# Kernel optimization log

Hardware: AMD Instinct MI355X
Metric: run time of the kernel (lower is better)

## Reference

```python
import jax, jax.numpy as jnp
import numpy as np

N = 50000      # nodes
E = 800000     # edges (before self-loops)
IN, HID, HEADS, OUT = 128, 16, 8, 64
NEG_SLOPE = 0.2
EPS = 1e-16


def gat_layer(x, edge_index, W, att_src, att_dst, bias, heads, ch, num_nodes, concat):
    # x: [N, F_in]; edge_index: [2, E'] (row0 = source j, row1 = target i)
    h = (x @ W).reshape(-1, heads, ch)                     # [N, H, C]
    a_src = jnp.sum(h * att_src, axis=-1)                  # [N, H]
    a_dst = jnp.sum(h * att_dst, axis=-1)                  # [N, H]
    src, dst = edge_index[0], edge_index[1]
    alpha = a_src[src] + a_dst[dst]                        # [E', H]
    alpha = jax.nn.leaky_relu(alpha, NEG_SLOPE)
    # segment softmax over incoming edges of each target node
    m = jax.ops.segment_max(alpha, dst, num_segments=num_nodes)
    alpha = jnp.exp(alpha - m[dst])
    denom = jax.ops.segment_sum(alpha, dst, num_segments=num_nodes)
    alpha = alpha / (denom[dst] + EPS)
    msg = h[src] * alpha[:, :, None]                       # [E', H, C]
    out = jax.ops.segment_sum(msg, dst, num_segments=num_nodes)  # [N, H, C]
    out = out.reshape(-1, heads * ch) if concat else out.mean(axis=1)
    return out + bias


def gat_model(x, edge_index, W1, att_src1, att_dst1, b1, W2, att_src2, att_dst2, b2, num_nodes):
    # PyG GATConv default add_self_loops=True
    loops = jnp.arange(num_nodes, dtype=edge_index.dtype)
    ei = jnp.concatenate([edge_index, jnp.stack([loops, loops])], axis=1)
    h = gat_layer(x, ei, W1, att_src1, att_dst1, b1, HEADS, HID, num_nodes, concat=True)
    h = jax.nn.relu(h)
    return gat_layer(h, ei, W2, att_src2, att_dst2, b2, 1, OUT, num_nodes, concat=False)


def setup_inputs() -> dict:
    key = jax.random.key(0)
    ks = jax.random.split(key, 10)
    x = jax.random.normal(ks[0], (N, IN), jnp.float32)
    edge_index = jax.random.randint(ks[1], (2, E), 0, N, dtype=jnp.int32)
    W1 = jax.random.normal(ks[2], (IN, HEADS * HID), jnp.float32) / np.sqrt(IN).astype(np.float32)
    att_src1 = jax.random.normal(ks[3], (HEADS, HID), jnp.float32) * 0.1
    att_dst1 = jax.random.normal(ks[4], (HEADS, HID), jnp.float32) * 0.1
    b1 = jnp.zeros((HEADS * HID,), jnp.float32)
    W2 = jax.random.normal(ks[5], (HEADS * HID, OUT), jnp.float32) / np.sqrt(HEADS * HID).astype(np.float32)
    att_src2 = jax.random.normal(ks[6], (1, OUT), jnp.float32) * 0.1
    att_dst2 = jax.random.normal(ks[7], (1, OUT), jnp.float32) * 0.1
    b2 = jnp.zeros((OUT,), jnp.float32)
    return {"x": x, "edge_index": edge_index, "W1": W1, "att_src1": att_src1,
            "att_dst1": att_dst1, "b1": b1, "W2": W2, "att_src2": att_src2,
            "att_dst2": att_dst2, "b2": b2, "num_nodes": N}


def reference(x, edge_index, W1, att_src1, att_dst1, b1, W2, att_src2, att_dst2, b2, num_nodes):
    return gat_model(x, edge_index, W1, att_src1, att_dst1, b1,
                     W2, att_src2, att_dst2, b2, num_nodes)
```

## Files before the change

### kernel.cpp

```cpp
#include <hip/hip_runtime.h>

#define NEG 0.2f
#define EPSV 1e-16f
#define EPB 4096
#define CAPN 64
#define CAPB (256 * 18)

typedef _Float16 h4 __attribute__((ext_vector_type(4)));
typedef _Float16 h8 __attribute__((ext_vector_type(8)));
typedef float f32x4 __attribute__((ext_vector_type(4)));

__device__ __forceinline__ float lrelu(float x) { return x > 0.f ? x : NEG * x; }

__global__ void k_setup(const float* __restrict__ W1, _Float16* __restrict__ Wt1,
                        const float* __restrict__ W2, _Float16* __restrict__ Wt2,
                        int* __restrict__ bcur, int nbuckets) {
  const int bid = blockIdx.x, tid = threadIdx.x;
  if (bid < 64) {
    int t = bid * 256 + tid;
    int c = t >> 7, k = t & 127;
    Wt1[t] = (_Float16)W1[k * 128 + c];
  } else if (bid < 96) {
    int t = (bid - 64) * 256 + tid;
    if (t < 64 * 128) {
      int c = t >> 7, k = t & 127;
      Wt2[t] = (_Float16)W2[k * 64 + c];
    }
  } else {
    if (tid < nbuckets) bcur[tid] = tid * CAPB;
  }
}

__global__ __launch_bounds__(256) void k_bin_gemm1(
    const int* __restrict__ src, const int* __restrict__ dst, int* __restrict__ bcur,
    unsigned* __restrict__ binned, int E, int nBinB, const float* __restrict__ X,
    const _Float16* __restrict__ Wt, const float* __restrict__ atts,
    const float* __restrict__ attd, _Float16* __restrict__ Hout,
    float* __restrict__ as_, float* __restrict__ ad_, int N) {
  constexpr int K = 128, XS = 136;
  __shared__ _Float16 xs[64 * XS];
  const int tid = threadIdx.x;

  if ((int)blockIdx.x < nBinB) {
    int* hist = (int*)xs;
    int* base = hist + 256;
    const int b0 = blockIdx.x * EPB;
    const int b1 = min(b0 + EPB, E);
    hist[tid] = 0;
    __syncthreads();
    for (int e = b0 + tid; e < b1; e += 256) atomicAdd(&hist[dst[e] >> 8], 1);
    __syncthreads();
    int h = hist[tid];
    if (h > 0) base[tid] = atomicAdd(&bcur[tid], h);
    __syncthreads();
    hist[tid] = 0;
    __syncthreads();
    for (int e = b0 + tid; e < b1; e += 256) {
      int d = dst[e];
      int bk = d >> 8;
      int pos = base[bk] + atomicAdd(&hist[bk], 1);
      binned[pos] = ((unsigned)(d & 255) << 16) | (unsigned)src[e];
    }
    return;
  }

  const int bid = blockIdx.x - nBinB;
  const int wv = tid >> 6, lane = tid & 63;
  const long row0 = (long)bid * 64;
  const int nrow = (int)min((long)64, (long)N - row0);

  for (int idx = tid; idx < 64 * (K / 4); idx += 256) {
    int r = idx >> 5, iw = idx & 31;
    float4 v = make_float4(0.f, 0.f, 0.f, 0.f);
    if (r < nrow) v = *(const float4*)&X[(row0 + r) * K + iw * 4];
    h4 o;
    o[0] = (_Float16)v.x;
    o[1] = (_Float16)v.y;
    o[2] = (_Float16)v.z;
    o[3] = (_Float16)v.w;
    *(h4*)&xs[r * XS + iw * 4] = o;
  }
  __syncthreads();

  const int rlo = lane & 15, khi = lane >> 4;
  h8 a[4];
#pragma unroll
  for (int kb = 0; kb < 4; kb++)
    a[kb] = *(const h8*)&xs[(wv * 16 + rlo) * XS + kb * 32 + khi * 8];
  __syncthreads();

  const int orow = wv * 16 + khi * 4;
#pragma unroll
  for (int n = 0; n < 8; n++) {
    f32x4 acc = {0.f, 0.f, 0.f, 0.f};
#pragma unroll
    for (int kb = 0; kb < 4; kb++) {
      h8 b = *(const h8*)&Wt[(n * 16 + rlo) * K + kb * 32 + khi * 8];
      acc = __builtin_amdgcn_mfma_f32_16x16x32_f16(a[kb], b, acc, 0, 0, 0);
    }
#pragma unroll
    for (int r = 0; r < 4; r++) {
      _Float16 hv = (_Float16)acc[r];
      xs[(orow + r) * XS + n * 16 + rlo] = hv;
      if (orow + r < nrow) Hout[(row0 + orow + r) * 128 + n * 16 + rlo] = hv;
    }
  }
  __syncthreads();
  for (int t = tid; t < 64 * 8; t += 256) {
    int r = t >> 3, h = t & 7;
    if (r < nrow) {
      const _Float16* hp = &xs[r * XS + h * 16];
      const float* sp = &atts[h * 16];
      const float* dp = &attd[h * 16];
      float s = 0.f, d = 0.f;
#pragma unroll
      for (int c = 0; c < 16; c++) {
        float v = (float)hp[c];
        s += v * sp[c];
        d += v * dp[c];
      }
      as_[(row0 + r) * 8 + h] = s;
      ad_[(row0 + r) * 8 + h] = d;
    }
  }
}

__global__ __launch_bounds__(256) void k_unbin(const unsigned* __restrict__ binned,
                                               const int* __restrict__ bcur,
                                               unsigned short* __restrict__ csr_src,
                                               int* __restrict__ deg, int N) {
  __shared__ int cnt[256];
  const int n0 = blockIdx.x << 8;
  const int start = blockIdx.x * CAPB;
  const int end = bcur[blockIdx.x];
  cnt[threadIdx.x] = 0;
  __syncthreads();
  for (int t = start + (int)threadIdx.x; t < end; t += 256) {
    unsigned v = binned[t];
    int dl = (int)(v >> 16);
    int pos = atomicAdd(&cnt[dl], 1);
    if (pos < CAPN) csr_src[(long)(n0 + dl) * CAPN + pos] = (unsigned short)(v & 0xFFFFu);
  }
  __syncthreads();
  int n = n0 + (int)threadIdx.x;
  if (n < N) deg[n] = min(cnt[threadIdx.x], CAPN);
}

template <int M, int H, int C, typename TX>
__global__ __launch_bounds__(256) void k_gemm_mfma(const TX* __restrict__ X,
                                                   const _Float16* __restrict__ Wt,
                                                   const float* __restrict__ atts,
                                                   const float* __restrict__ attd,
                                                   _Float16* __restrict__ Hout,
                                                   float* __restrict__ as_,
                                                   float* __restrict__ ad_, int N) {
  constexpr int K = 128, XS = 136;
  __shared__ _Float16 xs[64 * XS];
  const int tid = threadIdx.x;
  const int wv = tid >> 6, lane = tid & 63;
  const long row0 = (long)blockIdx.x * 64;
  const int nrow = (int)min((long)64, (long)N - row0);

  if constexpr (sizeof(TX) == 4) {
    for (int idx = tid; idx < 64 * (K / 4); idx += 256) {
      int r = idx >> 5, iw = idx & 31;
      float4 v = make_float4(0.f, 0.f, 0.f, 0.f);
      if (r < nrow) v = *(const float4*)&X[(row0 + r) * K + iw * 4];
      h4 o;
      o[0] = (_Float16)v.x;
      o[1] = (_Float16)v.y;
      o[2] = (_Float16)v.z;
      o[3] = (_Float16)v.w;
      *(h4*)&xs[r * XS + iw * 4] = o;
    }
  } else {
    for (int idx = tid; idx < 64 * (K / 8); idx += 256) {
      int r = idx >> 4, iw = idx & 15;
      h8 v = {};
      if (r < nrow) v = *(const h8*)&X[(row0 + r) * K + iw * 8];
      *(h8*)&xs[r * XS + iw * 8] = v;
    }
  }
  __syncthreads();

  const int rlo = lane & 15, khi = lane >> 4;
  h8 a[4];
#pragma unroll
  for (int kb = 0; kb < 4; kb++)
    a[kb] = *(const h8*)&xs[(wv * 16 + rlo) * XS + kb * 32 + khi * 8];
  __syncthreads();

  constexpr int NT = M / 16;
  const int orow = wv * 16 + khi * 4;
#pragma unroll
  for (int n = 0; n < NT; n++) {
    f32x4 acc = {0.f, 0.f, 0.f, 0.f};
#pragma unroll
    for (int kb = 0; kb < 4; kb++) {
      h8 b = *(const h8*)&Wt[(n * 16 + rlo) * K + kb * 32 + khi * 8];
      acc = __builtin_amdgcn_mfma_f32_16x16x32_f16(a[kb], b, acc, 0, 0, 0);
    }
#pragma unroll
    for (int r = 0; r < 4; r++) {
      _Float16 hv = (_Float16)acc[r];
      xs[(orow + r) * XS + n * 16 + rlo] = hv;
      if (orow + r < nrow)
        Hout[(row0 + orow + r) * M + n * 16 + rlo] = hv;
    }
  }
  __syncthreads();
  for (int t = tid; t < 64 * H; t += 256) {
    int r = t / H, h = t - r * H;
    if (r < nrow) {
      const _Float16* hp = &xs[r * XS + h * C];
      const float* sp = &atts[h * C];
      const float* dp = &attd[h * C];
      float s = 0.f, d = 0.f;
#pragma unroll
      for (int c = 0; c < C; c++) {
        float v = (float)hp[c];
        s += v * sp[c];
        d += v * dp[c];
      }
      as_[(row0 + r) * H + h] = s;
      ad_[(row0 + r) * H + h] = d;
    }
  }
}

__global__ __launch_bounds__(256) void k_node1(const int* __restrict__ deg_,
                                               const unsigned short* __restrict__ csr_src,
                                               const _Float16* __restrict__ Hf,
                                               const float* __restrict__ as_,
                                               const float* __restrict__ ad_,
                                               const float* __restrict__ bias,
                                               _Float16* __restrict__ out, int N) {
  const int wid = threadIdx.x >> 6, lane = threadIdx.x & 63;
  const int i = blockIdx.x * 4 + wid;
  if (i >= N) return;
  const long beg = (long)i * CAPN;
  const int deg = deg_[i];
  const int sub = lane >> 4, ln = lane & 15;
  const int f0 = ln * 8, hf = ln >> 1;

  const float adh = ad_[i * 8 + hf];
  const float pself = __expf(lrelu(as_[i * 8 + hf] + adh));
  float acc[8] = {0.f, 0.f, 0.f, 0.f, 0.f, 0.f, 0.f, 0.f};
  float sp = 0.f;

  int e = sub;
  for (; e + 4 < deg; e += 8) {
    int j0 = (int)csr_src[beg + e], j1 = (int)csr_src[beg + e + 4];
    float p0 = __expf(lrelu(as_[j0 * 8 + hf] + adh));
    float p1 = __expf(lrelu(as_[j1 * 8 + hf] + adh));
    h8 v0 = *(const h8*)&Hf[(long)j0 * 128 + f0];
    h8 v1 = *(const h8*)&Hf[(long)j1 * 128 + f0];
    sp += p0 + p1;
#pragma unroll
    for (int c = 0; c < 8; c++) acc[c] += p0 * (float)v0[c] + p1 * (float)v1[c];
  }
  for (; e < deg; e += 4) {
    int j = (int)csr_src[beg + e];
    float p = __expf(lrelu(as_[j * 8 + hf] + adh));
    h8 v = *(const h8*)&Hf[(long)j * 128 + f0];
    sp += p;
#pragma unroll
    for (int c = 0; c < 8; c++) acc[c] += p * (float)v[c];
  }
  if (sub == 0) {
    h8 hv = *(const h8*)&Hf[(long)i * 128 + f0];
#pragma unroll
    for (int c = 0; c < 8; c++) acc[c] += pself * (float)hv[c];
  }
  sp += __shfl_xor(sp, 16);
  sp += __shfl_xor(sp, 32);
  const float rd = 1.f / (sp + pself + EPSV);
#pragma unroll
  for (int c = 0; c < 8; c++) {
    acc[c] += __shfl_xor(acc[c], 16);
    acc[c] += __shfl_xor(acc[c], 32);
  }
  if (sub == 0) {
    h8 o;
#pragma unroll
    for (int c = 0; c < 8; c++)
      o[c] = (_Float16)fmaxf(acc[c] * rd + bias[f0 + c], 0.f);
    *(h8*)&out[(long)i * 128 + f0] = o;
  }
}

__global__ __launch_bounds__(256) void k_node2(const int* __restrict__ deg_,
                                               const unsigned short* __restrict__ csr_src,
                                               const _Float16* __restrict__ Hf,
                                               const float* __restrict__ as_,
                                               const float* __restrict__ ad_,
                                               const float* __restrict__ bias,
                                               float* __restrict__ out, int N) {
  const int wid = threadIdx.x >> 6, lane = threadIdx.x & 63;
  const int i = blockIdx.x * 4 + wid;
  if (i >= N) return;
  const long beg = (long)i * CAPN;
  const int deg = deg_[i];
  const int sub = lane >> 3, ln = lane & 7;
  const int f0 = ln * 8;

  const float adi = ad_[i];
  const float pself = __expf(lrelu(as_[i] + adi));
  float acc[8] = {0.f, 0.f, 0.f, 0.f, 0.f, 0.f, 0.f, 0.f};
  float sp = 0.f;

  int e = sub;
  for (; e + 8 < deg; e += 16) {
    int j0 = (int)csr_src[beg + e], j1 = (int)csr_src[beg + e + 8];
    float p0 = __expf(lrelu(as_[j0] + adi));
    float p1 = __expf(lrelu(as_[j1] + adi));
    h8 v0 = *(const h8*)&Hf[(long)j0 * 64 + f0];
    h8 v1 = *(const h8*)&Hf[(long)j1 * 64 + f0];
    sp += p0 + p1;
#pragma unroll
    for (int c = 0; c < 8; c++) acc[c] += p0 * (float)v0[c] + p1 * (float)v1[c];
  }
  for (; e < deg; e += 8) {
    int j = (int)csr_src[beg + e];
    float p = __expf(lrelu(as_[j] + adi));
    h8 v = *(const h8*)&Hf[(long)j * 64 + f0];
    sp += p;
#pragma unroll
    for (int c = 0; c < 8; c++) acc[c] += p * (float)v[c];
  }
  if (sub == 0) {
    h8 hv = *(const h8*)&Hf[(long)i * 64 + f0];
#pragma unroll
    for (int c = 0; c < 8; c++) acc[c] += pself * (float)hv[c];
  }
  sp += __shfl_xor(sp, 8);
  sp += __shfl_xor(sp, 16);
  sp += __shfl_xor(sp, 32);
  const float rd = 1.f / (sp + pself + EPSV);
#pragma unroll
  for (int c = 0; c < 8; c++) {
    acc[c] += __shfl_xor(acc[c], 8);
    acc[c] += __shfl_xor(acc[c], 16);
    acc[c] += __shfl_xor(acc[c], 32);
  }
  if (sub == 0) {
    float4 b0 = *(const float4*)&bias[f0];
    float4 b1 = *(const float4*)&bias[f0 + 4];
    float4 o0, o1;
    o0.x = acc[0] * rd + b0.x;
    o0.y = acc[1] * rd + b0.y;
    o0.z = acc[2] * rd + b0.z;
    o0.w = acc[3] * rd + b0.w;
    o1.x = acc[4] * rd + b1.x;
    o1.y = acc[5] * rd + b1.y;
    o1.z = acc[6] * rd + b1.z;
    o1.w = acc[7] * rd + b1.w;
    *(float4*)&out[(long)i * 64 + f0] = o0;
    *(float4*)&out[(long)i * 64 + f0 + 4] = o1;
  }
}

extern "C" void kernel_launch(void* const* d_in, const int* in_sizes, int n_in,
                              void* d_out, int out_size, void* d_ws, size_t ws_size,
                              hipStream_t stream) {
  const float* x = (const float*)d_in[0];
  const int* ei = (const int*)d_in[1];
  const float* W1 = (const float*)d_in[2];
  const float* s1 = (const float*)d_in[3];
  const float* dd1 = (const float*)d_in[4];
  const float* b1 = (const float*)d_in[5];
  const float* W2 = (const float*)d_in[6];
  const float* s2 = (const float*)d_in[7];
  const float* dd2 = (const float*)d_in[8];
  const float* b2 = (const float*)d_in[9];
  const int N = in_sizes[0] / 128;
  const int E = in_sizes[1] / 2;
  const int* src = ei;
  const int* dst = ei + E;
  const int nbuckets = (N + 255) >> 8;
  const int nBinB = (E + EPB - 1) / EPB;
  const int nGemmB = (N + 63) / 64;

  char* wsp = (char*)d_ws;
  _Float16* Wt1 = (_Float16*)wsp;
  _Float16* Wt2 = Wt1 + 128 * 128;
  _Float16* Hh = Wt2 + 64 * 128;
  float* as1 = (float*)((char*)Hh + (size_t)N * 128 * sizeof(_Float16));
  float* ad1 = as1 + (size_t)N * 8;
  _Float16* X2h = (_Float16*)(ad1 + (size_t)N * 8);
  int* deg = (int*)(X2h + (size_t)N * 128);
  unsigned short* csr_src = (unsigned short*)(deg + N);
  int* bcur = (int*)(csr_src + (size_t)N * CAPN);
  unsigned* binned = (unsigned*)(bcur + 256);
  float* out = (float*)d_out;

  dim3 B(256);

  k_setup<<<dim3(97), B, 0, stream>>>(W1, Wt1, W2, Wt2, bcur, nbuckets);

  k_bin_gemm1<<<dim3(nBinB + nGemmB), B, 0, stream>>>(
      src, dst, bcur, binned, E, nBinB, x, Wt1, s1, dd1, Hh, as1, ad1, N);

  k_unbin<<<dim3(nbuckets), B, 0, stream>>>(binned, bcur, csr_src, deg, N);

  k_node1<<<dim3((N + 3) / 4), B, 0, stream>>>(deg, csr_src, Hh, as1, ad1, b1, X2h, N);

  k_gemm_mfma<64, 1, 64, _Float16><<<dim3(nGemmB), B, 0, stream>>>(
      X2h, Wt2, s2, dd2, Hh, as1, ad1, N);

  k_node2<<<dim3((N + 3) / 4), B, 0, stream>>>(deg, csr_src, Hh, as1, ad1, b2, out, N);
}
```

Baseline: 126.4 us.

## Use finer 64-node buckets for edge binning with register-cached dst and nontemporal IO

Edge binning now uses 1024 buckets of 64 nodes instead of 196 buckets of 256 nodes. The unbin pass therefore runs many more, smaller blocks with better parallelism and a smaller scatter footprint. Each binning thread keeps its 16 dst values in registers so dst is not re-read, and binned writes and reads use nontemporal hints. Bucket counters become relative offsets zeroed by a memset, with an overflow guard at CAPB. The risk is more global atomic contention on the bucket counters and silently dropped edges if a bucket overflows.

```diff
diff --git a/kernel.cpp b/kernel.cpp
--- a/kernel.cpp
+++ b/kernel.cpp
@@ -4,7 +4,9 @@
 #define EPSV 1e-16f
 #define EPB 4096
 #define CAPN 64
-#define CAPB (256 * 18)
+#define BSH 6
+#define CAPB 1280
+#define NBK 1024
 
 typedef _Float16 h4 __attribute__((ext_vector_type(4)));
 typedef _Float16 h8 __attribute__((ext_vector_type(8)));
@@ -13,21 +15,18 @@
 __device__ __forceinline__ float lrelu(float x) { return x > 0.f ? x : NEG * x; }
 
 __global__ void k_setup(const float* __restrict__ W1, _Float16* __restrict__ Wt1,
-                        const float* __restrict__ W2, _Float16* __restrict__ Wt2,
-                        int* __restrict__ bcur, int nbuckets) {
+                        const float* __restrict__ W2, _Float16* __restrict__ Wt2) {
   const int bid = blockIdx.x, tid = threadIdx.x;
   if (bid < 64) {
     int t = bid * 256 + tid;
     int c = t >> 7, k = t & 127;
     Wt1[t] = (_Float16)W1[k * 128 + c];
-  } else if (bid < 96) {
+  } else {
     int t = (bid - 64) * 256 + tid;
     if (t < 64 * 128) {
       int c = t >> 7, k = t & 127;
       Wt2[t] = (_Float16)W2[k * 64 + c];
     }
-  } else {
-    if (tid < nbuckets) bcur[tid] = tid * CAPB;
   }
 }
 
@@ -43,23 +42,35 @@
 
   if ((int)blockIdx.x < nBinB) {
     int* hist = (int*)xs;
-    int* base = hist + 256;
+    int* base = hist + NBK;
     const int b0 = blockIdx.x * EPB;
-    const int b1 = min(b0 + EPB, E);
-    hist[tid] = 0;
+    int dv[16];
+    for (int s = tid; s < NBK; s += 256) hist[s] = 0;
     __syncthreads();
-    for (int e = b0 + tid; e < b1; e += 256) atomicAdd(&hist[dst[e] >> 8], 1);
+#pragma unroll
+    for (int t = 0; t < 16; t++) {
+      int e = b0 + t * 256 + tid;
+      dv[t] = (e < E) ? dst[e] : -1;
+      if (dv[t] >= 0) atomicAdd(&hist[dv[t] >> BSH], 1);
+    }
     __syncthreads();
-    int h = hist[tid];
-    if (h > 0) base[tid] = atomicAdd(&bcur[tid], h);
+    for (int s = tid; s < NBK; s += 256) {
+      int h = hist[s];
+      if (h > 0) base[s] = s * CAPB + atomicAdd(&bcur[s], h);
+      hist[s] = 0;
+    }
     __syncthreads();
-    hist[tid] = 0;
-    __syncthreads();
-    for (int e = b0 + tid; e < b1; e += 256) {
-      int d = dst[e];
-      int bk = d >> 8;
-      int pos = base[bk] + atomicAdd(&hist[bk], 1);
-      binned[pos] = ((unsigned)(d & 255) << 16) | (unsigned)src[e];
+#pragma unroll
+    for (int t = 0; t < 16; t++) {
+      if (dv[t] >= 0) {
+        int e = b0 + t * 256 + tid;
+        int bk = dv[t] >> BSH;
+        int off = atomicAdd(&hist[bk], 1);
+        int pos = base[bk] + off;
+        if (base[bk] + off < (bk + 1) * CAPB)
+          __builtin_nontemporal_store(
+              ((unsigned)(dv[t] & 63) << 16) | (unsigned)src[e], &binned[pos]);
+      }
     }
     return;
   }
@@ -129,21 +140,21 @@
                                                const int* __restrict__ bcur,
                                                unsigned short* __restrict__ csr_src,
                                                int* __restrict__ deg, int N) {
-  __shared__ int cnt[256];
-  const int n0 = blockIdx.x << 8;
+  __shared__ int cnt[64];
+  const int n0 = blockIdx.x << BSH;
   const int start = blockIdx.x * CAPB;
-  const int end = bcur[blockIdx.x];
-  cnt[threadIdx.x] = 0;
+  const int end = start + min(bcur[blockIdx.x], CAPB);
+  if (threadIdx.x < 64) cnt[threadIdx.x] = 0;
   __syncthreads();
   for (int t = start + (int)threadIdx.x; t < end; t += 256) {
-    unsigned v = binned[t];
+    unsigned v = __builtin_nontemporal_load(&binned[t]);
     int dl = (int)(v >> 16);
     int pos = atomicAdd(&cnt[dl], 1);
     if (pos < CAPN) csr_src[(long)(n0 + dl) * CAPN + pos] = (unsigned short)(v & 0xFFFFu);
   }
   __syncthreads();
   int n = n0 + (int)threadIdx.x;
-  if (n < N) deg[n] = min(cnt[threadIdx.x], CAPN);
+  if (threadIdx.x < 64 && n < N) deg[n] = min(cnt[threadIdx.x], CAPN);
 }
 
 template <int M, int H, int C, typename TX>
@@ -377,7 +388,7 @@
   const int E = in_sizes[1] / 2;
   const int* src = ei;
   const int* dst = ei + E;
-  const int nbuckets = (N + 255) >> 8;
+  const int nbuckets = (N + 63) >> BSH;
   const int nBinB = (E + EPB - 1) / EPB;
   const int nGemmB = (N + 63) / 64;
 
@@ -391,12 +402,13 @@
   int* deg = (int*)(X2h + (size_t)N * 128);
   unsigned short* csr_src = (unsigned short*)(deg + N);
   int* bcur = (int*)(csr_src + (size_t)N * CAPN);
-  unsigned* binned = (unsigned*)(bcur + 256);
+  unsigned* binned = (unsigned*)(bcur + 1024);
   float* out = (float*)d_out;
 
   dim3 B(256);
 
-  k_setup<<<dim3(97), B, 0, stream>>>(W1, Wt1, W2, Wt2, bcur, nbuckets);
+  hipMemsetAsync(bcur, 0, (size_t)nbuckets * sizeof(int), stream);
+  k_setup<<<dim3(96), B, 0, stream>>>(W1, Wt1, W2, Wt2);
 
   k_bin_gemm1<<<dim3(nBinB + nGemmB), B, 0, stream>>>(
       src, dst, bcur, binned, E, nBinB, x, Wt1, s1, dd1, Hh, as1, ad1, N);
```

Result: slower. 138.7 us (+9.7%).
